# Optimization experiments

Measured on AMD Instinct MI355X. Metric: run time of the kernel, lower is better.

Reference implementation:

```python
import jax, jax.numpy as jnp
import numpy as np

B, N, D = 64, 32, 512

# Off-diagonal pair indices in the exact order the torch module uses:
# k = N*i + j for i in range(N) for j in range(N) if j != i.
_pairs = [(i, j) for i in range(N) for j in range(N) if j != i]
IDX_I = jnp.asarray(np.array([p[0] for p in _pairs], dtype=np.int32))  # [N*(N-1)]
IDX_J = jnp.asarray(np.array([p[1] for p in _pairs], dtype=np.int32))


def setup_inputs() -> dict:
    key = jax.random.key(0)
    k0, k1, k2 = jax.random.split(key, 3)
    person_feats = jax.random.normal(k0, (B, N, D), dtype=jnp.float32)
    # MLP: Linear(2D -> D) -> ReLU -> Linear(D -> D); Kaiming-ish scaling.
    W1 = jax.random.normal(k1, (D, 2 * D), dtype=jnp.float32) * (1.0 / np.sqrt(2 * D))
    b1 = jnp.zeros((D,), dtype=jnp.float32)
    W2 = jax.random.normal(k2, (D, D), dtype=jnp.float32) * (1.0 / np.sqrt(D))
    b2 = jnp.zeros((D,), dtype=jnp.float32)
    return {"person_feats": person_feats, "W1": W1, "b1": b1, "W2": W2, "b2": b2}


def reference(person_feats, W1, b1, W2, b2):
    # Original math: tem1[b, N*i+j] = feats[b, i]; tem2[b, N*i+j] = feats[b, j];
    # select off-diagonal indices -> pairwise concat(feat_i, feat_j).
    # We gather the N*(N-1) needed pairs directly instead of materializing N*N.
    fi = person_feats[:, IDX_I, :]            # [B, N*(N-1), D]
    fj = person_feats[:, IDX_J, :]            # [B, N*(N-1), D]
    x = jnp.concatenate([fi, fj], axis=-1)    # [B, N*(N-1), 2D]
    h = jax.nn.relu(jnp.einsum('bpk,dk->bpd', x, W1) + b1)
    out = jnp.einsum('bpk,dk->bpd', h, W2) + b2  # [B, N*(N-1), D]
    return out
```

## Files before the change

kernel.cpp:

```cpp
#include <hip/hip_runtime.h>
#include <hip/hip_bf16.h>
#include <stdint.h>


typedef __attribute__((ext_vector_type(4))) float f32x4;
typedef __attribute__((ext_vector_type(8))) short bf16x8;
typedef __attribute__((ext_vector_type(4))) unsigned int u32x4;

__device__ __forceinline__ uint32_t cvt2_bf16(float a, float b) {
    __hip_bfloat162 h = __float22bfloat162_rn(make_float2(a, b));
    uint32_t u;
    __builtin_memcpy(&u, &h, 4);
    return u;
}

__global__ __launch_bounds__(256) void prep(const float* __restrict__ pf,
                                            const float* __restrict__ W1,
                                            const float* __restrict__ b1,
                                            const float* __restrict__ W2,
                                            unsigned short* __restrict__ UVb,
                                            unsigned short* __restrict__ W2r) {
    __shared__ unsigned short As[32][64];
    __shared__ unsigned short Bs[128][64];

    const int t = threadIdx.x;
    const int bxg = blockIdx.x;

    if (bxg >= 512) {
        int s = (bxg - 512) * 256 + t;
        int l = s & 63;
        int fn = (s >> 6) & 31;
        int kt = s >> 11;
        int col = fn * 16 + (l & 15);
        int k = kt * 32 + (l >> 4) * 8;
        const float* src = W2 + (size_t)col * 512 + k;
        f32x4 a = ((const f32x4*)src)[0];
        f32x4 b = ((const f32x4*)src)[1];
        u32x4 P;
        P[0] = cvt2_bf16(a[0], a[1]); P[1] = cvt2_bf16(a[2], a[3]);
        P[2] = cvt2_bf16(b[0], b[1]); P[3] = cvt2_bf16(b[2], b[3]);
        *(u32x4*)(W2r + (size_t)s * 8) = P;
        return;
    }

    const int m0 = (bxg >> 3) * 32;
    const int c0 = (bxg & 7) * 128;

    const int row8 = t >> 3;
    const int g = t & 7;

    const int wave = t >> 6, lane = t & 63;
    const int wr = wave >> 1, wc = wave & 1;
    const int lr = lane & 15, lkq = lane >> 4;
    const int s7 = lr & 7;

    f32x4 acc[4] = {};

    const float* a_src = pf + (size_t)(m0 + row8) * 512 + g * 8;
    const float* b_src[4];
    int wbB[4];
#pragma unroll
    for (int p = 0; p < 4; ++p) {
        int rb = p * 32 + row8;
        int c = c0 + rb;
        int d = c & 511;
        int koff = (c >> 9) * 512;
        b_src[p] = W1 + (size_t)d * 1024 + koff + g * 8;
        wbB[p] = rb * 128 + ((g ^ (rb & 7)) << 4);
    }
    const int wbA = row8 * 128 + ((g ^ (row8 & 7)) << 4);

    for (int kt = 0; kt < 512; kt += 64) {
        {
            const float* gp = a_src + kt;
            f32x4 x0 = ((const f32x4*)gp)[0];
            f32x4 x1 = ((const f32x4*)gp)[1];
            u32x4 P;
            P[0] = cvt2_bf16(x0[0], x0[1]); P[1] = cvt2_bf16(x0[2], x0[3]);
            P[2] = cvt2_bf16(x1[0], x1[1]); P[3] = cvt2_bf16(x1[2], x1[3]);
            *(u32x4*)((char*)&As[0][0] + wbA) = P;
        }
#pragma unroll
        for (int p = 0; p < 4; ++p) {
            const float* gp = b_src[p] + kt;
            f32x4 x0 = ((const f32x4*)gp)[0];
            f32x4 x1 = ((const f32x4*)gp)[1];
            u32x4 P;
            P[0] = cvt2_bf16(x0[0], x0[1]); P[1] = cvt2_bf16(x0[2], x0[3]);
            P[2] = cvt2_bf16(x1[0], x1[1]); P[3] = cvt2_bf16(x1[2], x1[3]);
            *(u32x4*)((char*)&Bs[0][0] + wbB[p]) = P;
        }
        __syncthreads();
#pragma unroll
        for (int kk = 0; kk < 2; ++kk) {
            const int co = (((kk << 2) + lkq) ^ s7) << 3;
            bf16x8 af = *(const bf16x8*)(&As[0][0] + (wr * 16 + lr) * 64 + co);
#pragma unroll
            for (int n = 0; n < 4; ++n) {
                bf16x8 bfr = *(const bf16x8*)(&Bs[0][0] + (wc * 64 + n * 16 + lr) * 64 + co);
                acc[n] = __builtin_amdgcn_mfma_f32_16x16x32_bf16(af, bfr, acc[n], 0, 0, 0);
            }
        }
        __syncthreads();
    }

    const int cr = lane >> 4;
    const int cc = lane & 15;
#pragma unroll
    for (int n = 0; n < 4; ++n) {
        int c = c0 + wc * 64 + n * 16 + cc;
        float bias = (c < 512) ? b1[c] : 0.0f;
        int rowb = m0 + wr * 16 + cr * 4;
#pragma unroll
        for (int r_ = 0; r_ < 4; ++r_)
            UVb[(size_t)(rowb + r_) * 1024 + c] =
                (unsigned short)(cvt2_bf16(acc[n][r_] + bias, 0.0f) & 0xFFFFu);
    }
}

__global__ __launch_bounds__(256, 2) void fused_gemm(const unsigned short* __restrict__ UVb,
                                                     const unsigned short* __restrict__ W2r,
                                                     const float* __restrict__ b2,
                                                     float* __restrict__ out) {
    __shared__ unsigned char As[4][4096];

    const int t = threadIdx.x;
    const int bx = blockIdx.x;
    const int mt = (bx & 7) * 124 + (bx >> 3);
    const int m0 = mt << 6;

    const int wave = t >> 6, lane = t & 63;

    const int arow = t >> 2;
    const int ks = t & 3;
    const unsigned short* uptr;
    const unsigned short* vptr;
    {
        int m = m0 + arow;
        int b = m / 992, p = m - b * 992;
        int i = p / 31, r = p - i * 31;
        int j = r + (r >= i ? 1 : 0);
        uptr = UVb + (size_t)(b * 32 + i) * 1024 + ks * 8;
        vptr = UVb + (size_t)(b * 32 + j) * 1024 + 512 + ks * 8;
    }
    const int awoff = (arow >> 4) * 1024 + (ks * 16 + (arow & 15)) * 16;

    const unsigned char* bsrc = (const unsigned char*)W2r +
                                (size_t)(wave * 8) * 1024 + lane * 16;

    const int cr = lane >> 4;
    const int cc = lane & 15;

    f32x4 acc[8][4] = {};

    u32x4 Pub, Pvb;
    u32x4 Qub, Qvb;
    bf16x8 Bp[8], Bq[8];

#define LOAD_B(S, DST)                                                         \
    {                                                                          \
        const unsigned char* gb = bsrc + (size_t)(S) * 32768;                  \
        _Pragma("unroll")                                                      \
        for (int n = 0; n < 8; ++n)                                            \
            DST[n] = *(const bf16x8*)(gb + n * 1024);                          \
    }

#define LOAD_UV(S, Ub, Vb)                                                     \
    {                                                                          \
        Ub = *(const u32x4*)(uptr + (S) * 32);                                 \
        Vb = *(const u32x4*)(vptr + (S) * 32);                                 \
    }

#define BUILD_A(DSTBUF, Ub, Vb)                                                \
    {                                                                          \
        u32x4 P;                                                               \
        _Pragma("unroll")                                                      \
        for (int q = 0; q < 4; ++q) {                                          \
            uint32_t uw = Ub[q], vw = Vb[q];                                   \
            uint32_t t0, t1;                                                   \
            float ul, uh, vl, vh;                                              \
            t0 = uw << 16; t1 = uw & 0xFFFF0000u;                              \
            __builtin_memcpy(&ul, &t0, 4); __builtin_memcpy(&uh, &t1, 4);      \
            t0 = vw << 16; t1 = vw & 0xFFFF0000u;                              \
            __builtin_memcpy(&vl, &t0, 4); __builtin_memcpy(&vh, &t1, 4);      \
            P[q] = cvt2_bf16(fmaxf(ul + vl, 0.0f), fmaxf(uh + vh, 0.0f));      \
        }                                                                      \
        *(u32x4*)(&As[DSTBUF][0] + awoff) = P;                                 \
    }

#define MFMA_STEP(BUF, BREG)                                                   \
    {                                                                          \
        const unsigned char* aB = &As[BUF][0];                                 \
        bf16x8 af[4];                                                          \
        _Pragma("unroll")                                                      \
        for (int m = 0; m < 4; ++m)                                            \
            af[m] = *(const bf16x8*)(aB + m * 1024 + lane * 16);               \
        __builtin_amdgcn_s_setprio(1);                                         \
        _Pragma("unroll")                                                      \
        for (int n = 0; n < 8; ++n)                                            \
            _Pragma("unroll")                                                  \
            for (int m = 0; m < 4; ++m)                                        \
                acc[n][m] = __builtin_amdgcn_mfma_f32_16x16x32_bf16(           \
                    af[m], BREG[n], acc[n][m], 0, 0, 0);                       \
        __builtin_amdgcn_s_setprio(0);                                         \
    }

#define BARRIER() asm volatile("s_waitcnt lgkmcnt(0)\n\ts_barrier" ::: "memory")

    LOAD_B(0, Bp);
    LOAD_B(1, Bq);
    LOAD_UV(0, Pub, Pvb);
    LOAD_UV(1, Qub, Qvb);
    BUILD_A(0, Pub, Pvb);
    BUILD_A(1, Qub, Qvb);

#pragma unroll 1
    for (int s2 = 0; s2 < 16; s2 += 2) {
        BARRIER();
        if (s2 < 14) {
            LOAD_UV(s2 + 2, Pub, Pvb);
            LOAD_UV(s2 + 3, Qub, Qvb);
        }
        MFMA_STEP(s2 & 3, Bp);
        if (s2 < 14) LOAD_B(s2 + 2, Bp);
        MFMA_STEP((s2 + 1) & 3, Bq);
        if (s2 < 14) {
            LOAD_B(s2 + 3, Bq);
            BUILD_A((s2 + 2) & 3, Pub, Pvb);
            BUILD_A((s2 + 3) & 3, Qub, Qvb);
        }
    }
#undef LOAD_B
#undef LOAD_UV
#undef BUILD_A
#undef MFMA_STEP
#undef BARRIER

#pragma unroll
    for (int n = 0; n < 8; ++n) {
        int col = wave * 128 + n * 16 + cc;
        float bias = b2[col];
#pragma unroll
        for (int m = 0; m < 4; ++m) {
            int rowb = m0 + m * 16 + cr * 4;
#pragma unroll
            for (int r_ = 0; r_ < 4; ++r_)
                out[(size_t)(rowb + r_) * 512 + col] = acc[n][m][r_] + bias;
        }
    }
}

extern "C" void kernel_launch(void* const* d_in, const int* in_sizes, int n_in,
                              void* d_out, int out_size, void* d_ws, size_t ws_size,
                              hipStream_t stream) {
    const float* pf = (const float*)d_in[0];
    const float* W1 = (const float*)d_in[1];
    const float* b1 = (const float*)d_in[2];
    const float* W2 = (const float*)d_in[3];
    const float* b2 = (const float*)d_in[4];
    float* out = (float*)d_out;

    unsigned short* UVb = (unsigned short*)d_ws;
    unsigned short* W2r = (unsigned short*)((char*)d_ws + (size_t)8 * 1024 * 1024);

    prep<<<dim3(640), dim3(256), 0, stream>>>(pf, W1, b1, W2, UVb, W2r);
    fused_gemm<<<dim3(992), dim3(256), 0, stream>>>(UVb, W2r, b2, out);
}
```

Measured before the change: 68.01 us.

## Deepen A-tile LDS ring to 8 stages and process four k-steps per barrier

Doubles the shared-memory A staging ring from 4 to 8 slots and prebuilds four k-steps up front. The main loop now covers four MFMA steps per barrier instead of two, which halves the number of block-wide barriers and gives global UV loads more time in flight before they are consumed. In exchange, LDS use rises to 32KB per block, which could limit occupancy beyond the 2 blocks per CU requested by the launch bounds, and it adds register pressure from the longer unrolled body.

```diff
diff --git a/kernel.cpp b/kernel.cpp
--- a/kernel.cpp
+++ b/kernel.cpp
@@ -122,7 +122,7 @@
                                                      const unsigned short* __restrict__ W2r,
                                                      const float* __restrict__ b2,
                                                      float* __restrict__ out) {
-    __shared__ unsigned char As[4][4096];
+    __shared__ unsigned char As[8][4096];
 
     const int t = threadIdx.x;
     const int bx = blockIdx.x;
@@ -213,21 +213,35 @@
     LOAD_UV(1, Qub, Qvb);
     BUILD_A(0, Pub, Pvb);
     BUILD_A(1, Qub, Qvb);
+    LOAD_UV(2, Pub, Pvb);
+    LOAD_UV(3, Qub, Qvb);
+    BUILD_A(2, Pub, Pvb);
+    BUILD_A(3, Qub, Qvb);
 
 #pragma unroll 1
-    for (int s2 = 0; s2 < 16; s2 += 2) {
+    for (int s4 = 0; s4 < 16; s4 += 4) {
         BARRIER();
-        if (s2 < 14) {
-            LOAD_UV(s2 + 2, Pub, Pvb);
-            LOAD_UV(s2 + 3, Qub, Qvb);
-        }
-        MFMA_STEP(s2 & 3, Bp);
-        if (s2 < 14) LOAD_B(s2 + 2, Bp);
-        MFMA_STEP((s2 + 1) & 3, Bq);
-        if (s2 < 14) {
-            LOAD_B(s2 + 3, Bq);
-            BUILD_A((s2 + 2) & 3, Pub, Pvb);
-            BUILD_A((s2 + 3) & 3, Qub, Qvb);
+        if (s4 < 12) {
+            LOAD_UV(s4 + 4, Pub, Pvb);
+            LOAD_UV(s4 + 5, Qub, Qvb);
+        }
+        MFMA_STEP(s4 & 7, Bp);
+        LOAD_B(s4 + 2, Bp);
+        MFMA_STEP((s4 + 1) & 7, Bq);
+        LOAD_B(s4 + 3, Bq);
+        if (s4 < 12) {
+            BUILD_A((s4 + 4) & 7, Pub, Pvb);
+            BUILD_A((s4 + 5) & 7, Qub, Qvb);
+            LOAD_UV(s4 + 6, Pub, Pvb);
+            LOAD_UV(s4 + 7, Qub, Qvb);
+        }
+        MFMA_STEP((s4 + 2) & 7, Bp);
+        if (s4 < 12) LOAD_B(s4 + 4, Bp);
+        MFMA_STEP((s4 + 3) & 7, Bq);
+        if (s4 < 12) {
+            LOAD_B(s4 + 5, Bq);
+            BUILD_A((s4 + 6) & 7, Pub, Pvb);
+            BUILD_A((s4 + 7) & 7, Qub, Qvb);
         }
     }
 #undef LOAD_B
```

Measured after the change: 102.1 us. 1.5x slower.
